# Optimization experiments

Hardware: AMD Instinct MI355X
Metric: run time of the kernel (lower is better)

## Reference

```python
import jax, jax.numpy as jnp
import numpy as np

B, N, D, S, H, ITERS = 64, 4096, 128, 7, 256, 3
EPS = 1e-8

def layer_norm(x, g, b):
    m = jnp.mean(x, axis=-1, keepdims=True)
    v = jnp.var(x, axis=-1, keepdims=True)
    return (x - m) * jax.lax.rsqrt(v + 1e-5) * g + b

def setup_inputs() -> dict:
    key = jax.random.key(0)
    ks = jax.random.split(key, 16)
    lin = lambda k, o, i: jax.random.normal(k, (o, i), jnp.float32) / np.sqrt(i)
    return {
        "embeddings": jax.random.normal(ks[0], (B, N, D), jnp.float32),
        "noise": jax.random.normal(ks[1], (B, S, D), jnp.float32),
        "slots_mu": jax.random.normal(ks[2], (1, 1, D), jnp.float32),
        "slots_sigma": jax.random.uniform(ks[3], (1, 1, D), jnp.float32),
        "Wk": lin(ks[4], D, D), "bk": jnp.zeros((D,), jnp.float32),
        "Wq": lin(ks[5], D, D), "bq": jnp.zeros((D,), jnp.float32),
        "Wv": lin(ks[6], D, D), "bv": jnp.zeros((D,), jnp.float32),
        "W_ih": lin(ks[7], 3 * D, D), "W_hh": lin(ks[8], 3 * D, D),
        "b_ih": jnp.zeros((3 * D,), jnp.float32), "b_hh": jnp.zeros((3 * D,), jnp.float32),
        "W1": lin(ks[9], H, D), "b1": jnp.zeros((H,), jnp.float32),
        "W2": lin(ks[10], D, H), "b2": jnp.zeros((D,), jnp.float32),
        "ln_in_g": jnp.ones((D,), jnp.float32), "ln_in_b": jnp.zeros((D,), jnp.float32),
        "ln_s_g": jnp.ones((D,), jnp.float32), "ln_s_b": jnp.zeros((D,), jnp.float32),
        "ln_ff_g": jnp.ones((D,), jnp.float32), "ln_ff_b": jnp.zeros((D,), jnp.float32),
    }

def reference(embeddings, noise, slots_mu, slots_sigma, Wk, bk, Wq, bq, Wv, bv,
              W_ih, W_hh, b_ih, b_hh, W1, b1, W2, b2,
              ln_in_g, ln_in_b, ln_s_g, ln_s_b, ln_ff_g, ln_ff_b):
    # slot init: normal(mu, sigma) with fixed noise
    slots = slots_mu + slots_sigma * noise  # [B,S,D]
    emb = layer_norm(embeddings, ln_in_g, ln_in_b)
    keys = emb @ Wk.T + bk      # [B,N,D]
    values = emb @ Wv.T + bv    # [B,N,D]
    for _ in range(ITERS):
        slots_prev = slots
        q = layer_norm(slots, ln_s_g, ln_s_b) @ Wq.T + bq  # [B,S,D]
        dots = jnp.einsum('bid,bjd->bij', q, keys)          # [B,S,N]
        attn = jax.nn.softmax(dots, axis=-1) + EPS
        attn = attn / jnp.sum(attn, axis=-1, keepdims=True)
        updates = jnp.einsum('bjd,bij->bid', values, attn)  # [B,S,D]
        # GRUCell (pytorch gate order: r, z, n)
        x = updates.reshape(-1, D)
        h = slots_prev.reshape(-1, D)
        gi = x @ W_ih.T + b_ih
        gh = h @ W_hh.T + b_hh
        gi_r, gi_z, gi_n = jnp.split(gi, 3, axis=-1)
        gh_r, gh_z, gh_n = jnp.split(gh, 3, axis=-1)
        r = jax.nn.sigmoid(gi_r + gh_r)
        z = jax.nn.sigmoid(gi_z + gh_z)
        n = jnp.tanh(gi_n + r * gh_n)
        slots = ((1.0 - z) * n + z * h).reshape(B, S, D)
        ff = jax.nn.relu(layer_norm(slots, ln_ff_g, ln_ff_b) @ W1.T + b1) @ W2.T + b2
        slots = slots + ff
    return slots
```

## Files before the change

kernel.cpp:

```cpp
#include <hip/hip_runtime.h>
#include <math.h>

#define B_ 64
#define N_ 4096
#define D_ 128
#define S_ 7
#define H_ 256
#define ITERS_ 3
#define AP 132
#define NCHUNK 8

__device__ __forceinline__ float dot4(float4 a, float4 b) {
  return a.x * b.x + a.y * b.y + a.z * b.z + a.w * b.w;
}
__device__ __forceinline__ float4 ld4(const float* p) {
  return *reinterpret_cast<const float4*>(p);
}

__global__ void k_init(const float* __restrict__ noise, const float* __restrict__ mu,
                       const float* __restrict__ sigma, float* __restrict__ slots) {
  int idx = blockIdx.x * 256 + threadIdx.x;
  int d = idx & 127;
  slots[idx] = mu[d] + sigma[d] * noise[idx];
}

__global__ __launch_bounds__(128) void k_q(
    const float* __restrict__ slots, const float* __restrict__ Wq, const float* __restrict__ bq,
    const float* __restrict__ g, const float* __restrict__ b,
    const float* __restrict__ Wk, float* __restrict__ qp) {
  __shared__ __align__(16) float lns[AP];
  __shared__ __align__(16) float qs2[AP];
  __shared__ float red[4];
  int row = blockIdx.x;
  int d = threadIdx.x;
  float x = slots[row * D_ + d];
  float s1 = x, s2 = x * x;
#pragma unroll
  for (int off = 32; off >= 1; off >>= 1) { s1 += __shfl_down(s1, off); s2 += __shfl_down(s2, off); }
  if ((d & 63) == 0) { red[(d >> 6) * 2] = s1; red[(d >> 6) * 2 + 1] = s2; }
  __syncthreads();
  float sum = red[0] + red[2], sumsq = red[1] + red[3];
  float mean = sum * (1.f / 128.f);
  float var = sumsq * (1.f / 128.f) - mean * mean;
  float rs = rsqrtf(var + 1e-5f);
  lns[d] = (x - mean) * rs * g[d] + b[d];
  __syncthreads();
  const float* w = Wq + d * D_;
  float acc = bq[d];
  for (int i4 = 0; i4 < D_; i4 += 4) acc += dot4(*reinterpret_cast<const float4*>(&lns[i4]), ld4(w + i4));
  qs2[d] = acc;
  __syncthreads();
  float qpa = 0.f;
#pragma unroll 4
  for (int dd = 0; dd < D_; dd++) qpa += qs2[dd] * Wk[dd * D_ + d];
  qp[row * D_ + d] = qpa;
}

__global__ __launch_bounds__(256) void k_attn(
    const float* __restrict__ qpbuf, const float* __restrict__ emb,
    const float* __restrict__ lng, const float* __restrict__ lnb,
    float* __restrict__ partialA, float* __restrict__ partialM, float* __restrict__ partialS) {
  __shared__ __align__(16) float qs[7 * AP];
  __shared__ __align__(16) float vt[64 * AP];
  __shared__ float red[28 * 64];
  __shared__ float pt[7 * 64];
  __shared__ float sm[7], ssum[7], tmax[7];
  int t = threadIdx.x;
  int b = blockIdx.x >> 3, jc = blockIdx.x & (NCHUNK - 1);

  if (t < 224) {
    int s = t >> 5, i4 = (t & 31) * 4;
    *reinterpret_cast<float4*>(&qs[s * AP + i4]) = ld4(&qpbuf[(b * 7 + s) * D_ + i4]);
  }
  if (t < 7) { sm[t] = -1e30f; ssum[t] = 0.f; }

  int j = t & 63, g = t >> 6, ib = g * 32;
  int d4 = (t & 31) * 4, jg = t >> 5;
  int ln_i4 = (t & 31) * 4;
  int ln_r8 = t >> 5;
  float4 gv = ld4(&lng[ln_i4]);
  float4 bv4 = ld4(&lnb[ln_i4]);

  float acc[7][4];
#pragma unroll
  for (int s = 0; s < 7; s++)
#pragma unroll
    for (int c = 0; c < 4; c++) acc[s][c] = 0.f;
  __syncthreads();

  for (int sub = 0; sub < 8; sub++) {
    int j0 = jc * 512 + sub * 64;
#pragma unroll
    for (int u = 0; u < 8; u++) {
      int row = u * 8 + ln_r8;
      float4 x = ld4(&emb[((long)b * N_ + j0 + row) * D_ + ln_i4]);
      float s1 = x.x + x.y + x.z + x.w;
      float s2 = dot4(x, x);
#pragma unroll
      for (int off = 16; off >= 1; off >>= 1) {
        s1 += __shfl_xor(s1, off, 32);
        s2 += __shfl_xor(s2, off, 32);
      }
      float mean = s1 * (1.f / 128.f);
      float var = s2 * (1.f / 128.f) - mean * mean;
      float rs = rsqrtf(var + 1e-5f);
      float4 o;
      o.x = (x.x - mean) * rs * gv.x + bv4.x;
      o.y = (x.y - mean) * rs * gv.y + bv4.y;
      o.z = (x.z - mean) * rs * gv.z + bv4.z;
      o.w = (x.w - mean) * rs * gv.w + bv4.w;
      *reinterpret_cast<float4*>(&vt[row * AP + ln_i4]) = o;
    }
    __syncthreads();

    float acc7[7];
#pragma unroll
    for (int s = 0; s < 7; s++) acc7[s] = 0.f;
#pragma unroll
    for (int st = 0; st < 8; st++) {
      float4 kv = *reinterpret_cast<const float4*>(&vt[j * AP + ib + st * 4]);
#pragma unroll
      for (int s = 0; s < 7; s++) {
        float4 qv = *reinterpret_cast<const float4*>(&qs[s * AP + ib + st * 4]);
        acc7[s] += dot4(kv, qv);
      }
    }
#pragma unroll
    for (int s = 0; s < 7; s++) red[(g * 7 + s) * 64 + j] = acc7[s];
    __syncthreads();

    for (int pp = t; pp < 448; pp += 256) {
      int s = pp >> 6, jj = pp & 63;
      pt[pp] = red[s * 64 + jj] + red[(7 + s) * 64 + jj] +
               red[(14 + s) * 64 + jj] + red[(21 + s) * 64 + jj];
    }
    __syncthreads();

    if (t < 224) {
      int s = t >> 5, i = t & 31;
      float m = fmaxf(pt[s * 64 + i], pt[s * 64 + 32 + i]);
#pragma unroll
      for (int off = 16; off >= 1; off >>= 1) m = fmaxf(m, __shfl_down(m, off, 32));
      if ((t & 31) == 0) tmax[s] = m;
    }
    __syncthreads();

#pragma unroll
    for (int s = 0; s < 7; s++) {
      float mnew = fmaxf(sm[s], tmax[s]);
      float scl = __expf(sm[s] - mnew);
#pragma unroll
      for (int c = 0; c < 4; c++) acc[s][c] *= scl;
    }
    for (int pp = t; pp < 448; pp += 256) {
      int s = pp >> 6;
      float mnew = fmaxf(sm[s], tmax[s]);
      pt[pp] = __expf(pt[pp] - mnew);
    }
    __syncthreads();

    if (t < 224) {
      int s = t >> 5, i = t & 31;
      float ssub = pt[s * 64 + i] + pt[s * 64 + 32 + i];
#pragma unroll
      for (int off = 16; off >= 1; off >>= 1) ssub += __shfl_down(ssub, off, 32);
      if ((t & 31) == 0) {
        float mnew = fmaxf(sm[s], tmax[s]);
        float scl = __expf(sm[s] - mnew);
        ssum[s] = ssum[s] * scl + ssub;
        sm[s] = mnew;
      }
    }

#pragma unroll
    for (int jl = 0; jl < 8; jl++) {
      int jj = jg * 8 + jl;
      float4 vv = *reinterpret_cast<const float4*>(&vt[jj * AP + d4]);
#pragma unroll
      for (int s = 0; s < 7; s++) {
        float e = pt[s * 64 + jj];
        acc[s][0] += e * vv.x; acc[s][1] += e * vv.y;
        acc[s][2] += e * vv.z; acc[s][3] += e * vv.w;
      }
    }
    __syncthreads();
  }

  float* redf = vt;
#pragma unroll
  for (int s = 0; s < 7; s++)
    *reinterpret_cast<float4*>(&redf[(jg * 7 + s) * 128 + d4]) =
        make_float4(acc[s][0], acc[s][1], acc[s][2], acc[s][3]);
  __syncthreads();
  for (int pp = t; pp < 896; pp += 256) {
    int s = pp >> 7, d = pp & 127;
    float x = 0.f;
#pragma unroll
    for (int g2 = 0; g2 < 8; g2++) x += redf[(g2 * 7 + s) * 128 + d];
    partialA[((long)(b * NCHUNK + jc) * 7 + s) * 128 + d] = x;
  }
  if (t < 7) {
    partialM[(b * NCHUNK + jc) * 7 + t] = sm[t];
    partialS[(b * NCHUNK + jc) * 7 + t] = ssum[t];
  }
}

__global__ __launch_bounds__(256) void k_gruffq(
    const float* __restrict__ partialA, const float* __restrict__ partialM,
    const float* __restrict__ partialS, float* __restrict__ slots,
    const float* __restrict__ Wv, const float* __restrict__ bv,
    const float* __restrict__ Wih, const float* __restrict__ Whh,
    const float* __restrict__ bih, const float* __restrict__ bhh,
    const float* __restrict__ W1, const float* __restrict__ b1,
    const float* __restrict__ W2, const float* __restrict__ b2,
    const float* __restrict__ gff, const float* __restrict__ bff,
    const float* __restrict__ lsg, const float* __restrict__ lsb,
    const float* __restrict__ Wq, const float* __restrict__ bq,
    const float* __restrict__ Wk, float* __restrict__ qp, int compute_q) {
  __shared__ __align__(16) float us[AP];
  __shared__ __align__(16) float xs[AP];
  __shared__ __align__(16) float hs[AP];
  __shared__ __align__(16) float nss[AP];
  __shared__ __align__(16) float lns[AP];
  __shared__ __align__(16) float sn[AP];
  __shared__ __align__(16) float qv[AP];
  __shared__ __align__(16) float h1s[H_];
  __shared__ __align__(16) float g6[6 * 128];
  __shared__ __align__(16) float pp[2 * 128];
  __shared__ float den2[2];
  __shared__ float red2[2];
  int t = threadIdx.x;
  int d = t & 127, h = t >> 7;
  int blk = blockIdx.x;
  int b = blk / 7, s = blk % 7;

  float mg = -1e30f;
#pragma unroll
  for (int c = 0; c < NCHUNK; c++) mg = fmaxf(mg, partialM[(b * NCHUNK + c) * 7 + s]);
  float up = 0.f, den = 0.f;
#pragma unroll
  for (int cc = 0; cc < NCHUNK / 2; cc++) {
    int c = h * (NCHUNK / 2) + cc;
    float w = __expf(partialM[(b * NCHUNK + c) * 7 + s] - mg);
    den += w * partialS[(b * NCHUNK + c) * 7 + s];
    up += w * partialA[((long)(b * NCHUNK + c) * 7 + s) * 128 + d];
  }
  pp[h * 128 + d] = up;
  if (d == 0) den2[h] = den;
  if (h == 1) hs[d] = slots[blk * D_ + d];
  __syncthreads();
  if (h == 0) us[d] = (pp[d] + pp[128 + d]) / (den2[0] + den2[1]);
  __syncthreads();

  {
    const float* wvr = Wv + d * D_ + h * 64;
    float acc = 0.f;
    for (int i4 = 0; i4 < 64; i4 += 4)
      acc += dot4(*reinterpret_cast<const float4*>(&us[h * 64 + i4]), ld4(wvr + i4));
    pp[h * 128 + d] = acc;
  }
  __syncthreads();
  if (h == 0) xs[d] = bv[d] + pp[d] + pp[128 + d];
  __syncthreads();

  {
    const float* base = (h == 0) ? Wih : Whh;
    const float* bias = (h == 0) ? bih : bhh;
    const float* vec = (h == 0) ? xs : hs;
    float a0 = bias[d], a1 = bias[128 + d], a2 = bias[256 + d];
    const float* w0 = base + d * D_;
    const float* w1 = base + (128 + d) * D_;
    const float* w2 = base + (256 + d) * D_;
    for (int i4 = 0; i4 < D_; i4 += 4) {
      float4 v = *reinterpret_cast<const float4*>(&vec[i4]);
      a0 += dot4(v, ld4(w0 + i4));
      a1 += dot4(v, ld4(w1 + i4));
      a2 += dot4(v, ld4(w2 + i4));
    }
    g6[(h * 3 + 0) * 128 + d] = a0;
    g6[(h * 3 + 1) * 128 + d] = a1;
    g6[(h * 3 + 2) * 128 + d] = a2;
  }
  __syncthreads();
  if (h == 0) {
    float gir = g6[d], giz = g6[128 + d], gin = g6[256 + d];
    float ghr = g6[384 + d], ghz = g6[512 + d], ghn = g6[640 + d];
    float r = 1.f / (1.f + __expf(-(gir + ghr)));
    float z = 1.f / (1.f + __expf(-(giz + ghz)));
    float n = tanhf(gin + r * ghn);
    nss[d] = (1.f - z) * n + z * hs[d];
  }
  __syncthreads();

  if (t < 64) {
    float v0 = nss[t], v1 = nss[t + 64];
    float s1 = v0 + v1, s2 = v0 * v0 + v1 * v1;
#pragma unroll
    for (int off = 32; off >= 1; off >>= 1) { s1 += __shfl_down(s1, off); s2 += __shfl_down(s2, off); }
    if (t == 0) { red2[0] = s1; red2[1] = s2; }
  }
  __syncthreads();
  {
    float mean = red2[0] * (1.f / 128.f);
    float var = red2[1] * (1.f / 128.f) - mean * mean;
    float rs = rsqrtf(var + 1e-5f);
    if (h == 0) lns[d] = (nss[d] - mean) * rs * gff[d] + bff[d];
  }
  __syncthreads();

  {
    float a = b1[t];
    const float* w = W1 + t * D_;
    for (int i4 = 0; i4 < D_; i4 += 4)
      a += dot4(*reinterpret_cast<const float4*>(&lns[i4]), ld4(w + i4));
    h1s[t] = fmaxf(a, 0.f);
  }
  __syncthreads();

  {
    const float* w2r = W2 + d * H_ + h * 128;
    float acc = 0.f;
    for (int h4 = 0; h4 < 128; h4 += 4)
      acc += dot4(*reinterpret_cast<const float4*>(&h1s[h * 128 + h4]), ld4(w2r + h4));
    pp[h * 128 + d] = acc;
  }
  __syncthreads();
  if (h == 0) {
    float out = nss[d] + b2[d] + pp[d] + pp[128 + d];
    sn[d] = out;
    slots[blk * D_ + d] = out;
  }
  __syncthreads();

  if (!compute_q) return;

  if (t < 64) {
    float v0 = sn[t], v1 = sn[t + 64];
    float s1 = v0 + v1, s2 = v0 * v0 + v1 * v1;
#pragma unroll
    for (int off = 32; off >= 1; off >>= 1) { s1 += __shfl_down(s1, off); s2 += __shfl_down(s2, off); }
    if (t == 0) { red2[0] = s1; red2[1] = s2; }
  }
  __syncthreads();
  {
    float mean = red2[0] * (1.f / 128.f);
    float var = red2[1] * (1.f / 128.f) - mean * mean;
    float rs = rsqrtf(var + 1e-5f);
    if (h == 0) lns[d] = (sn[d] - mean) * rs * lsg[d] + lsb[d];
  }
  __syncthreads();
  {
    const float* w = Wq + d * D_ + h * 64;
    float acc = 0.f;
    for (int i4 = 0; i4 < 64; i4 += 4)
      acc += dot4(*reinterpret_cast<const float4*>(&lns[h * 64 + i4]), ld4(w + i4));
    pp[h * 128 + d] = acc;
  }
  __syncthreads();
  if (h == 0) qv[d] = bq[d] + pp[d] + pp[128 + d];
  __syncthreads();
  {
    float acc = 0.f;
    const float* wc = Wk + h * 64 * D_ + d;
#pragma unroll 4
    for (int dd = 0; dd < 64; dd++) acc += qv[h * 64 + dd] * wc[dd * D_];
    pp[h * 128 + d] = acc;
  }
  __syncthreads();
  if (h == 0) qp[blk * D_ + d] = pp[d] + pp[128 + d];
}

extern "C" void kernel_launch(void* const* d_in, const int* in_sizes, int n_in,
                              void* d_out, int out_size, void* d_ws, size_t ws_size,
                              hipStream_t stream) {
  const float* emb   = (const float*)d_in[0];
  const float* noise = (const float*)d_in[1];
  const float* mu    = (const float*)d_in[2];
  const float* sigma = (const float*)d_in[3];
  const float* Wk = (const float*)d_in[4];  const float* bk = (const float*)d_in[5];
  const float* Wq = (const float*)d_in[6];  const float* bq = (const float*)d_in[7];
  const float* Wv = (const float*)d_in[8];  const float* bv = (const float*)d_in[9];
  const float* Wih = (const float*)d_in[10]; const float* Whh = (const float*)d_in[11];
  const float* bih = (const float*)d_in[12]; const float* bhh = (const float*)d_in[13];
  const float* W1 = (const float*)d_in[14];  const float* b1 = (const float*)d_in[15];
  const float* W2 = (const float*)d_in[16];  const float* b2 = (const float*)d_in[17];
  const float* lin_g = (const float*)d_in[18]; const float* lin_b = (const float*)d_in[19];
  const float* ls_g  = (const float*)d_in[20]; const float* ls_b  = (const float*)d_in[21];
  const float* lff_g = (const float*)d_in[22]; const float* lff_b = (const float*)d_in[23];
  (void)bk;

  float* slots = (float*)d_out;
  float* qp       = (float*)d_ws;
  float* partialA = qp + (size_t)B_ * S_ * D_;
  float* partialM = partialA + (size_t)B_ * NCHUNK * S_ * D_;
  float* partialS = partialM + (size_t)B_ * NCHUNK * S_;

  k_init<<<224, 256, 0, stream>>>(noise, mu, sigma, slots);
  k_q<<<448, 128, 0, stream>>>(slots, Wq, bq, ls_g, ls_b, Wk, qp);
  for (int it = 0; it < ITERS_; it++) {
    k_attn<<<B_ * NCHUNK, 256, 0, stream>>>(qp, emb, lin_g, lin_b, partialA, partialM, partialS);
    k_gruffq<<<448, 256, 0, stream>>>(partialA, partialM, partialS, slots, Wv, bv,
                                      Wih, Whh, bih, bhh, W1, b1, W2, b2, lff_g, lff_b,
                                      ls_g, ls_b, Wq, bq, Wk, qp, it < ITERS_ - 1 ? 1 : 0);
  }
}
```

Measured before the change: 537.2 us.

## Double attention block width and prefetch next embedding tile into registers

```diff
diff --git a/kernel.cpp b/kernel.cpp
--- a/kernel.cpp
+++ b/kernel.cpp
@@ -56,13 +56,13 @@
   qp[row * D_ + d] = qpa;
 }
 
-__global__ __launch_bounds__(256) void k_attn(
+__global__ __launch_bounds__(512) void k_attn(
     const float* __restrict__ qpbuf, const float* __restrict__ emb,
     const float* __restrict__ lng, const float* __restrict__ lnb,
     float* __restrict__ partialA, float* __restrict__ partialM, float* __restrict__ partialS) {
   __shared__ __align__(16) float qs[7 * AP];
   __shared__ __align__(16) float vt[64 * AP];
-  __shared__ float red[28 * 64];
+  __shared__ float red[56 * 64];
   __shared__ float pt[7 * 64];
   __shared__ float sm[7], ssum[7], tmax[7];
   int t = threadIdx.x;
@@ -74,26 +74,31 @@
   }
   if (t < 7) { sm[t] = -1e30f; ssum[t] = 0.f; }
 
-  int j = t & 63, g = t >> 6, ib = g * 32;
-  int d4 = (t & 31) * 4, jg = t >> 5;
+  int j = t & 63, g = t >> 6, ib = g * 16;
+  int d2 = (t & 63) * 2, jg = t >> 6;
   int ln_i4 = (t & 31) * 4;
-  int ln_r8 = t >> 5;
+  int ln_r = t >> 5;
   float4 gv = ld4(&lng[ln_i4]);
   float4 bv4 = ld4(&lnb[ln_i4]);
 
-  float acc[7][4];
-#pragma unroll
-  for (int s = 0; s < 7; s++)
-#pragma unroll
-    for (int c = 0; c < 4; c++) acc[s][c] = 0.f;
+  float acc[7][2];
+#pragma unroll
+  for (int s = 0; s < 7; s++) { acc[s][0] = 0.f; acc[s][1] = 0.f; }
+
+  float4 xr[4];
+  {
+    int j0 = jc * 512;
+#pragma unroll
+    for (int u = 0; u < 4; u++)
+      xr[u] = ld4(&emb[((long)b * N_ + j0 + u * 16 + ln_r) * D_ + ln_i4]);
+  }
   __syncthreads();
 
   for (int sub = 0; sub < 8; sub++) {
-    int j0 = jc * 512 + sub * 64;
-#pragma unroll
-    for (int u = 0; u < 8; u++) {
-      int row = u * 8 + ln_r8;
-      float4 x = ld4(&emb[((long)b * N_ + j0 + row) * D_ + ln_i4]);
+#pragma unroll
+    for (int u = 0; u < 4; u++) {
+      int row = u * 16 + ln_r;
+      float4 x = xr[u];
       float s1 = x.x + x.y + x.z + x.w;
       float s2 = dot4(x, x);
 #pragma unroll
@@ -113,11 +118,18 @@
     }
     __syncthreads();
 
+    if (sub < 7) {
+      int j0n = jc * 512 + (sub + 1) * 64;
+#pragma unroll
+      for (int u = 0; u < 4; u++)
+        xr[u] = ld4(&emb[((long)b * N_ + j0n + u * 16 + ln_r) * D_ + ln_i4]);
+    }
+
     float acc7[7];
 #pragma unroll
     for (int s = 0; s < 7; s++) acc7[s] = 0.f;
 #pragma unroll
-    for (int st = 0; st < 8; st++) {
+    for (int st = 0; st < 4; st++) {
       float4 kv = *reinterpret_cast<const float4*>(&vt[j * AP + ib + st * 4]);
 #pragma unroll
       for (int s = 0; s < 7; s++) {
@@ -129,10 +141,12 @@
     for (int s = 0; s < 7; s++) red[(g * 7 + s) * 64 + j] = acc7[s];
     __syncthreads();
 
-    for (int pp = t; pp < 448; pp += 256) {
-      int s = pp >> 6, jj = pp & 63;
-      pt[pp] = red[s * 64 + jj] + red[(7 + s) * 64 + jj] +
-               red[(14 + s) * 64 + jj] + red[(21 + s) * 64 + jj];
+    if (t < 448) {
+      int s = t >> 6, jj = t & 63;
+      float l = 0.f;
+#pragma unroll
+      for (int gg = 0; gg < 8; gg++) l += red[(gg * 7 + s) * 64 + jj];
+      pt[t] = l;
     }
     __syncthreads();
 
@@ -149,13 +163,12 @@
     for (int s = 0; s < 7; s++) {
       float mnew = fmaxf(sm[s], tmax[s]);
       float scl = __expf(sm[s] - mnew);
-#pragma unroll
-      for (int c = 0; c < 4; c++) acc[s][c] *= scl;
-    }
-    for (int pp = t; pp < 448; pp += 256) {
-      int s = pp >> 6;
+      acc[s][0] *= scl; acc[s][1] *= scl;
+    }
+    if (t < 448) {
+      int s = t >> 6;
       float mnew = fmaxf(sm[s], tmax[s]);
-      pt[pp] = __expf(pt[pp] - mnew);
+      pt[t] = __expf(pt[t] - mnew);
     }
     __syncthreads();
 
@@ -175,12 +188,11 @@
 #pragma unroll
     for (int jl = 0; jl < 8; jl++) {
       int jj = jg * 8 + jl;
-      float4 vv = *reinterpret_cast<const float4*>(&vt[jj * AP + d4]);
+      float2 vv = *reinterpret_cast<const float2*>(&vt[jj * AP + d2]);
 #pragma unroll
       for (int s = 0; s < 7; s++) {
         float e = pt[s * 64 + jj];
         acc[s][0] += e * vv.x; acc[s][1] += e * vv.y;
-        acc[s][2] += e * vv.z; acc[s][3] += e * vv.w;
       }
     }
     __syncthreads();
@@ -189,10 +201,10 @@
   float* redf = vt;
 #pragma unroll
   for (int s = 0; s < 7; s++)
-    *reinterpret_cast<float4*>(&redf[(jg * 7 + s) * 128 + d4]) =
-        make_float4(acc[s][0], acc[s][1], acc[s][2], acc[s][3]);
-  __syncthreads();
-  for (int pp = t; pp < 896; pp += 256) {
+    *reinterpret_cast<float2*>(&redf[(jg * 7 + s) * 128 + d2]) =
+        make_float2(acc[s][0], acc[s][1]);
+  __syncthreads();
+  for (int pp = t; pp < 896; pp += 512) {
     int s = pp >> 7, d = pp & 127;
     float x = 0.f;
 #pragma unroll
@@ -398,7 +410,7 @@
   k_init<<<224, 256, 0, stream>>>(noise, mu, sigma, slots);
   k_q<<<448, 128, 0, stream>>>(slots, Wq, bq, ls_g, ls_b, Wk, qp);
   for (int it = 0; it < ITERS_; it++) {
-    k_attn<<<B_ * NCHUNK, 256, 0, stream>>>(qp, emb, lin_g, lin_b, partialA, partialM, partialS);
+    k_attn<<<B_ * NCHUNK, 512, 0, stream>>>(qp, emb, lin_g, lin_b, partialA, partialM, partialS);
     k_gruffq<<<448, 256, 0, stream>>>(partialA, partialM, partialS, slots, Wv, bv,
                                       Wih, Whh, bih, bhh, W1, b1, W2, b2, lff_g, lff_b,
                                       ls_g, ls_b, Wq, bq, Wk, qp, it < ITERS_ - 1 ? 1 : 0);
```

Measured after the change: 550.1 us. +2.4%, slower.
